# Optimization experiments

Hardware: AMD Instinct MI355X
Metric: run time of the kernel (lower is better)

The kernel has to match this reference:

```python
import jax, jax.numpy as jnp
import numpy as np

N_NODES = 100000
N_EDGES = 600000
DIMS = [128, 64, 32, 16, 9]  # in_channels -> conv1 -> conv2 -> conv3 -> n_classes


def _sage_layer(x, src, dst, w_l, w_r, b, n_nodes):
    # PyG SAGEConv (mean aggr): out = lin_l(mean_{j in N(i)} x_j) + lin_r(x_i)
    msgs = x[src]                                               # [E, F] gather
    agg = jax.ops.segment_sum(msgs, dst, num_segments=n_nodes)  # [N, F]
    deg = jax.ops.segment_sum(jnp.ones((src.shape[0], 1), x.dtype), dst,
                              num_segments=n_nodes)             # [N, 1]
    agg = agg / jnp.maximum(deg, 1.0)                           # mean over neighbors
    return agg @ w_l + x @ w_r + b                              # lin_l has bias, lin_r does not


def setup_inputs() -> dict:
    key = jax.random.key(0)
    ks = jax.random.split(key, 16)
    inp = {
        'embedding': jax.random.normal(ks[0], (N_NODES, DIMS[0]), dtype=jnp.float32),
        'edge_index': jax.random.randint(ks[1], (2, N_EDGES), 0, N_NODES, dtype=jnp.int32),
        'edge_attr': jax.random.uniform(ks[2], (N_EDGES,), dtype=jnp.float32),
    }
    for i in range(4):
        fin, fout = DIMS[i], DIMS[i + 1]
        s = 1.0 / np.sqrt(fin)
        inp[f'w_l{i}'] = jax.random.uniform(ks[3 + 3 * i], (fin, fout), minval=-s, maxval=s, dtype=jnp.float32)
        inp[f'w_r{i}'] = jax.random.uniform(ks[4 + 3 * i], (fin, fout), minval=-s, maxval=s, dtype=jnp.float32)
        inp[f'b{i}'] = jax.random.uniform(ks[5 + 3 * i], (fout,), minval=-s, maxval=s, dtype=jnp.float32)
    return inp


def reference(embedding, edge_index, edge_attr,
              w_l0, w_r0, b0, w_l1, w_r1, b1,
              w_l2, w_r2, b2, w_l3, w_r3, b3):
    # edge_attr is accepted but unused: PyG SAGEConv does not consume edge weights.
    # Dropout evaluated in inference mode (identity) for a deterministic reference.
    src, dst = edge_index[0], edge_index[1]
    n = embedding.shape[0]
    x = jax.nn.relu(_sage_layer(embedding, src, dst, w_l0, w_r0, b0, n))
    x = jax.nn.relu(_sage_layer(x, src, dst, w_l1, w_r1, b1, n))
    x = jax.nn.relu(_sage_layer(x, src, dst, w_l2, w_r2, b2, n))
    x = _sage_layer(x, src, dst, w_l3, w_r3, b3, n)
    return x
```

## Files before the change

kernel.cpp:

```cpp
#include <hip/hip_runtime.h>
#include <hip/hip_bf16.h>


#define BLK 256


__global__ void hist_kernel(const int* __restrict__ dst, int* __restrict__ deg, int e) {
    int t = blockIdx.x * blockDim.x + threadIdx.x;
    if (t < e) atomicAdd(&deg[dst[t]], 1);
}

__global__ void scan1_kernel(const int* __restrict__ deg, int* __restrict__ excl,
                             int* __restrict__ bsums, int n) {
    __shared__ int sm[256];
    int base = blockIdx.x * 1024;
    int t = threadIdx.x;
    int v[4];
    int s = 0;
    #pragma unroll
    for (int j = 0; j < 4; j++) {
        int i = base + t * 4 + j;
        v[j] = (i < n) ? deg[i] : 0;
        s += v[j];
    }
    sm[t] = s;
    __syncthreads();
    for (int off = 1; off < 256; off <<= 1) {
        int x = (t >= off) ? sm[t - off] : 0;
        __syncthreads();
        sm[t] += x;
        __syncthreads();
    }
    int excl_t = sm[t] - s;
    if (t == 255) bsums[blockIdx.x] = sm[255];
    int run = excl_t;
    #pragma unroll
    for (int j = 0; j < 4; j++) {
        int i = base + t * 4 + j;
        if (i < n) excl[i] = run;
        run += v[j];
    }
}

__global__ void scan2_kernel(int* __restrict__ bsums, int nb) {
    __shared__ int sm[256];
    int t = threadIdx.x;
    int v = (t < nb) ? bsums[t] : 0;
    sm[t] = v;
    __syncthreads();
    for (int off = 1; off < 256; off <<= 1) {
        int x = (t >= off) ? sm[t - off] : 0;
        __syncthreads();
        sm[t] += x;
        __syncthreads();
    }
    if (t < nb) bsums[t] = sm[t] - v;
}

__global__ void scan3_kernel(const int* __restrict__ deg, int* __restrict__ row_start,
                             const int* __restrict__ bsums, int* __restrict__ cursor,
                             float* __restrict__ inv_deg, int n, int e) {
    int t = blockIdx.x * blockDim.x + threadIdx.x;
    if (t < n) {
        int rs = row_start[t] + bsums[t >> 10];
        row_start[t] = rs;
        cursor[t] = rs;
        int d = deg[t];
        inv_deg[t] = 1.0f / (float)(d > 1 ? d : 1);
    }
    if (t == 0) row_start[n] = e;
}

__global__ void scatter_kernel(const int* __restrict__ src, const int* __restrict__ dst,
                               int* __restrict__ cursor, int* __restrict__ ssrc, int e) {
    int t = blockIdx.x * blockDim.x + threadIdx.x;
    if (t < e) {
        int p = atomicAdd(&cursor[dst[t]], 1);
        ssrc[p] = src[t];
    }
}


template <int FIN, int FOUT, int BM, int KC, int TM, int TN, int THREADS>
__global__ void lin_tiled3(const float* __restrict__ x, const float* __restrict__ wl,
                           const float* __restrict__ wr, const float* __restrict__ b,
                           float* __restrict__ y, float* __restrict__ z, int n) {
    constexpr int PAD = 4;
    constexpr int CPR = FOUT / TN;
    constexpr int XLOADS = (BM * KC) / (THREADS * 4);
    static_assert(THREADS == (BM / TM) * CPR, "thread shape mismatch");
    __shared__ float xT[KC][BM + PAD];

    const int tid = threadIdx.x;
    const int r = tid / CPR;
    const int c = tid % CPR;
    const int m0 = r * TM;
    const int f0 = c * TN;
    const int nodeBase = blockIdx.x * BM;

    int nodeIdx[XLOADS], kkIdx[XLOADS];
    bool inb[XLOADS];
    #pragma unroll
    for (int l = 0; l < XLOADS; l++) {
        int idx = (l * THREADS + tid) * 4;
        nodeIdx[l] = idx / KC;
        kkIdx[l] = idx % KC;
        inb[l] = (nodeBase + nodeIdx[l]) < n;
    }

    float4 xreg[XLOADS];
    #pragma unroll
    for (int l = 0; l < XLOADS; l++) {
        float4 v = {0.f, 0.f, 0.f, 0.f};
        if (inb[l]) v = *(const float4*)(x + (size_t)(nodeBase + nodeIdx[l]) * FIN + kkIdx[l]);
        xreg[l] = v;
    }

    float accy[TM][TN] = {};
    float accz[TM][TN] = {};

    constexpr int NCHUNK = FIN / KC;
    for (int ch = 0; ch < NCHUNK; ch++) {
        #pragma unroll
        for (int l = 0; l < XLOADS; l++) {
            xT[kkIdx[l] + 0][nodeIdx[l]] = xreg[l].x;
            xT[kkIdx[l] + 1][nodeIdx[l]] = xreg[l].y;
            xT[kkIdx[l] + 2][nodeIdx[l]] = xreg[l].z;
            xT[kkIdx[l] + 3][nodeIdx[l]] = xreg[l].w;
        }
        __syncthreads();
        if (ch + 1 < NCHUNK) {
            int k0n = (ch + 1) * KC;
            #pragma unroll
            for (int l = 0; l < XLOADS; l++) {
                float4 v = {0.f, 0.f, 0.f, 0.f};
                if (inb[l]) v = *(const float4*)(x + (size_t)(nodeBase + nodeIdx[l]) * FIN + k0n + kkIdx[l]);
                xreg[l] = v;
            }
        }
        const int k0 = ch * KC;
        #pragma unroll 8
        for (int k = 0; k < KC; k++) {
            float a[TM];
            #pragma unroll
            for (int i = 0; i < TM; i += 4) *(float4*)&a[i] = *(const float4*)&xT[k][m0 + i];
            float4 blv = *(const float4*)(wl + (size_t)(k0 + k) * FOUT + f0);
            float4 brv = *(const float4*)(wr + (size_t)(k0 + k) * FOUT + f0);
            float bl[4] = {blv.x, blv.y, blv.z, blv.w};
            float br[4] = {brv.x, brv.y, brv.z, brv.w};
            #pragma unroll
            for (int i = 0; i < TM; i++)
                #pragma unroll
                for (int j = 0; j < TN; j++) {
                    accy[i][j] = fmaf(a[i], bl[j], accy[i][j]);
                    accz[i][j] = fmaf(a[i], br[j], accz[i][j]);
                }
        }
        __syncthreads();
    }

    float4 bv = *(const float4*)(b + f0);
    float bias[4] = {bv.x, bv.y, bv.z, bv.w};
    #pragma unroll
    for (int i = 0; i < TM; i++) {
        int gn = nodeBase + m0 + i;
        if (gn < n) {
            #pragma unroll
            for (int j = 0; j < TN; j += 4) {
                float4 vy = {accy[i][j], accy[i][j+1], accy[i][j+2], accy[i][j+3]};
                float4 vz = {accz[i][j] + bias[j], accz[i][j+1] + bias[j+1],
                             accz[i][j+2] + bias[j+2], accz[i][j+3] + bias[j+3]};
                *(float4*)(y + (size_t)gn * FOUT + f0 + j) = vy;
                *(float4*)(z + (size_t)gn * FOUT + f0 + j) = vz;
            }
        }
    }
}

template <int FIN, int FOUT>
__global__ void lin_naive(const float* __restrict__ x, const float* __restrict__ wl,
                          const float* __restrict__ wr, const float* __restrict__ b,
                          float* __restrict__ y, float* __restrict__ z, int n) {
    int t = blockIdx.x * blockDim.x + threadIdx.x;
    int node = t / FOUT;
    int f = t % FOUT;
    if (node >= n) return;
    const float* xr = x + (size_t)node * FIN;
    float accy = 0.f, accz = 0.f;
    #pragma unroll
    for (int k = 0; k < FIN; k++) {
        float xv = xr[k];
        accy = fmaf(xv, wl[k * FOUT + f], accy);
        accz = fmaf(xv, wr[k * FOUT + f], accz);
    }
    y[(size_t)node * FOUT + f] = accy;
    z[(size_t)node * FOUT + f] = accz + b[f];
}


template <int FOUT, bool RELU>
__global__ void agg4_kernel(const float4* __restrict__ y4, const int* __restrict__ row_start,
                            const int* __restrict__ ssrc, const float* __restrict__ inv_deg,
                            float4* __restrict__ out4, int n) {
    constexpr int Q = FOUT / 4;
    int t = blockIdx.x * blockDim.x + threadIdx.x;
    int node = t / Q;
    int q = t % Q;
    if (node >= n) return;
    int e0 = row_start[node];
    int e1 = row_start[node + 1];
    float4 s = {0.f, 0.f, 0.f, 0.f};
    int e = e0;
    for (; e + 3 < e1; e += 4) {
        int sn0 = ssrc[e];
        int sn1 = ssrc[e + 1];
        int sn2 = ssrc[e + 2];
        int sn3 = ssrc[e + 3];
        float4 v0 = y4[(size_t)sn0 * Q + q];
        float4 v1 = y4[(size_t)sn1 * Q + q];
        float4 v2 = y4[(size_t)sn2 * Q + q];
        float4 v3 = y4[(size_t)sn3 * Q + q];
        s.x += v0.x + v1.x + v2.x + v3.x;
        s.y += v0.y + v1.y + v2.y + v3.y;
        s.z += v0.z + v1.z + v2.z + v3.z;
        s.w += v0.w + v1.w + v2.w + v3.w;
    }
    if (e + 1 < e1) {
        int sn0 = ssrc[e];
        int sn1 = ssrc[e + 1];
        float4 v0 = y4[(size_t)sn0 * Q + q];
        float4 v1 = y4[(size_t)sn1 * Q + q];
        s.x += v0.x + v1.x; s.y += v0.y + v1.y;
        s.z += v0.z + v1.z; s.w += v0.w + v1.w;
        e += 2;
    }
    if (e < e1) {
        int sn = ssrc[e];
        float4 v = y4[(size_t)sn * Q + q];
        s.x += v.x; s.y += v.y; s.z += v.z; s.w += v.w;
    }
    float id = inv_deg[node];
    float4 o = out4[(size_t)node * Q + q];
    o.x += s.x * id; o.y += s.y * id; o.z += s.z * id; o.w += s.w * id;
    if (RELU) {
        o.x = fmaxf(o.x, 0.f); o.y = fmaxf(o.y, 0.f);
        o.z = fmaxf(o.z, 0.f); o.w = fmaxf(o.w, 0.f);
    }
    out4[(size_t)node * Q + q] = o;
}

template <int FOUT, bool RELU>
__global__ void agg_kernel(const float* __restrict__ y, const int* __restrict__ row_start,
                           const int* __restrict__ ssrc, const float* __restrict__ inv_deg,
                           float* __restrict__ out, int n) {
    int t = blockIdx.x * blockDim.x + threadIdx.x;
    int node = t / FOUT;
    int f = t % FOUT;
    if (node >= n) return;
    int e0 = row_start[node];
    int e1 = row_start[node + 1];
    float s = 0.f;
    int e = e0;
    for (; e + 3 < e1; e += 4) {
        int sn0 = ssrc[e];
        int sn1 = ssrc[e + 1];
        int sn2 = ssrc[e + 2];
        int sn3 = ssrc[e + 3];
        float v0 = y[(size_t)sn0 * FOUT + f];
        float v1 = y[(size_t)sn1 * FOUT + f];
        float v2 = y[(size_t)sn2 * FOUT + f];
        float v3 = y[(size_t)sn3 * FOUT + f];
        s += (v0 + v1) + (v2 + v3);
    }
    for (; e < e1; e++) s += y[(size_t)ssrc[e] * FOUT + f];
    float v = out[(size_t)node * FOUT + f] + s * inv_deg[node];
    if (RELU) v = fmaxf(v, 0.f);
    out[(size_t)node * FOUT + f] = v;
}


static inline int cdiv(int a, int b) { return (a + b - 1) / b; }

extern "C" void kernel_launch(void* const* d_in, const int* in_sizes, int n_in,
                              void* d_out, int out_size, void* d_ws, size_t ws_size,
                              hipStream_t stream) {
    const float* emb  = (const float*)d_in[0];
    const int*   eidx = (const int*)d_in[1];
    const float* wl0 = (const float*)d_in[3];
    const float* wr0 = (const float*)d_in[4];
    const float* b0  = (const float*)d_in[5];
    const float* wl1 = (const float*)d_in[6];
    const float* wr1 = (const float*)d_in[7];
    const float* b1  = (const float*)d_in[8];
    const float* wl2 = (const float*)d_in[9];
    const float* wr2 = (const float*)d_in[10];
    const float* b2  = (const float*)d_in[11];
    const float* wl3 = (const float*)d_in[12];
    const float* wr3 = (const float*)d_in[13];
    const float* b3  = (const float*)d_in[14];

    const int n = in_sizes[0] / 128;
    const int e = in_sizes[1] / 2;
    const int* src = eidx;
    const int* dst = eidx + e;

    char* ws = (char*)d_ws;
    size_t off = 0;
    auto alloc = [&](size_t bytes) -> void* {
        void* p = ws + off;
        off = (off + bytes + 255) & ~(size_t)255;
        return p;
    };
    int*   deg       = (int*)alloc((size_t)n * 4);
    float* inv_deg   = (float*)alloc((size_t)n * 4);
    int*   row_start = (int*)alloc(((size_t)n + 1) * 4);
    int*   cursor    = (int*)alloc((size_t)n * 4);
    int*   bsums     = (int*)alloc(1024 * 4);
    int*   ssrc      = (int*)alloc((size_t)e * 4);
    float* Y         = (float*)alloc((size_t)n * 64 * 4);
    float* xA        = (float*)alloc((size_t)n * 64 * 4);
    float* xB        = (float*)alloc((size_t)n * 32 * 4);
    (void)ws_size;

    hipMemsetAsync(deg, 0, (size_t)n * 4, stream);
    hist_kernel<<<cdiv(e, BLK), BLK, 0, stream>>>(dst, deg, e);
    int nchunks = cdiv(n, 1024);
    scan1_kernel<<<nchunks, 256, 0, stream>>>(deg, row_start, bsums, n);
    scan2_kernel<<<1, 256, 0, stream>>>(bsums, nchunks);
    scan3_kernel<<<cdiv(n, BLK), BLK, 0, stream>>>(deg, row_start, bsums, cursor, inv_deg, n, e);
    scatter_kernel<<<cdiv(e, BLK), BLK, 0, stream>>>(src, dst, cursor, ssrc, e);

    float* out = (float*)d_out;

    lin_tiled3<128, 64, 128, 32, 8, 4, 256><<<cdiv(n, 128), 256, 0, stream>>>(emb, wl0, wr0, b0, Y, xA, n);
    agg4_kernel<64, true><<<cdiv(n * 16, BLK), BLK, 0, stream>>>((const float4*)Y, row_start, ssrc, inv_deg, (float4*)xA, n);

    lin_tiled3<64, 32, 64, 32, 4, 4, 128><<<cdiv(n, 64), 128, 0, stream>>>(xA, wl1, wr1, b1, Y, xB, n);
    agg4_kernel<32, true><<<cdiv(n * 8, BLK), BLK, 0, stream>>>((const float4*)Y, row_start, ssrc, inv_deg, (float4*)xB, n);

    lin_naive<32, 16><<<cdiv(n * 16, BLK), BLK, 0, stream>>>(xB, wl2, wr2, b2, Y, xA, n);
    agg4_kernel<16, true><<<cdiv(n * 4, BLK), BLK, 0, stream>>>((const float4*)Y, row_start, ssrc, inv_deg, (float4*)xA, n);

    lin_naive<16, 9><<<cdiv(n * 9, BLK), BLK, 0, stream>>>(xA, wl3, wr3, b3, Y, out, n);
    agg_kernel<9, false><<<cdiv(n * 9, BLK), BLK, 0, stream>>>(Y, row_start, ssrc, inv_deg, out, n);
}
```

Baseline: 408.3 us.

## Use direct global-to-LDS async loads with double buffering in dense layer kernels

Replaces the register-staged transposed shared-memory tile in the two large linear kernels with __builtin_amdgcn_global_load_lds copies into a double-buffered row-major LDS tile, prefetching the next K chunk while computing the current one. Reads of x from LDS become per-row float4 loads instead of transposed column reads. The second layer now uses 128-node blocks with 256 threads, and launch bounds are fixed to one block per CU hint. The change is meant to cut VGPR staging and the transpose stores, but it risks LDS bank conflicts on row-major reads and relies on implicit ordering of the async LDS loads. Out-of-range rows are simply skipped rather than zero-filled, which leaves stale LDS data that only feeds accumulators for rows that are never stored.

Measured after the change: 417.9 us. 2.4% more time.

```diff
diff --git a/kernel.cpp b/kernel.cpp
--- a/kernel.cpp
+++ b/kernel.cpp
@@ -3,6 +3,11 @@
 
 
 #define BLK 256
+
+#define GLOAD_LDS16(gptr, lptr)                                              \
+    __builtin_amdgcn_global_load_lds(                                        \
+        (const __attribute__((address_space(1))) void*)(gptr),               \
+        (__attribute__((address_space(3))) void*)(lptr), 16, 0, 0)
 
 
 __global__ void hist_kernel(const int* __restrict__ dst, int* __restrict__ deg, int e) {
@@ -81,98 +86,88 @@
 }
 
 
-template <int FIN, int FOUT, int BM, int KC, int TM, int TN, int THREADS>
-__global__ void lin_tiled3(const float* __restrict__ x, const float* __restrict__ wl,
-                           const float* __restrict__ wr, const float* __restrict__ b,
-                           float* __restrict__ y, float* __restrict__ z, int n) {
-    constexpr int PAD = 4;
+template <int FIN, int FOUT, int BM, int KC, int TM, int THREADS>
+__global__ __launch_bounds__(THREADS, 1)
+void lin_glds(const float* __restrict__ x, const float* __restrict__ wl,
+              const float* __restrict__ wr, const float* __restrict__ b,
+              float* __restrict__ y, float* __restrict__ z, int n) {
+    constexpr int TN = 4;
     constexpr int CPR = FOUT / TN;
-    constexpr int XLOADS = (BM * KC) / (THREADS * 4);
     static_assert(THREADS == (BM / TM) * CPR, "thread shape mismatch");
-    __shared__ float xT[KC][BM + PAD];
+    constexpr int SLOTS = BM * KC / 4;
+    constexpr int LPT = SLOTS / THREADS;
+    constexpr int SPR = KC / 4;
+    constexpr int NCH = FIN / KC;
+    __shared__ float xs[2][BM * KC];
 
     const int tid = threadIdx.x;
+    const int wave = tid >> 6;
     const int r = tid / CPR;
     const int c = tid % CPR;
     const int m0 = r * TM;
-    const int f0 = c * TN;
     const int nodeBase = blockIdx.x * BM;
-
-    int nodeIdx[XLOADS], kkIdx[XLOADS];
-    bool inb[XLOADS];
-    #pragma unroll
-    for (int l = 0; l < XLOADS; l++) {
-        int idx = (l * THREADS + tid) * 4;
-        nodeIdx[l] = idx / KC;
-        kkIdx[l] = idx % KC;
-        inb[l] = (nodeBase + nodeIdx[l]) < n;
-    }
-
-    float4 xreg[XLOADS];
-    #pragma unroll
-    for (int l = 0; l < XLOADS; l++) {
-        float4 v = {0.f, 0.f, 0.f, 0.f};
-        if (inb[l]) v = *(const float4*)(x + (size_t)(nodeBase + nodeIdx[l]) * FIN + kkIdx[l]);
-        xreg[l] = v;
-    }
+    const float4* wl4 = (const float4*)wl;
+    const float4* wr4 = (const float4*)wr;
+
+    auto stage = [&](int buf, int ch) {
+        #pragma unroll
+        for (int l = 0; l < LPT; l++) {
+            int s = l * THREADS + tid;
+            int node = s / SPR;
+            int kq = s % SPR;
+            const float* g = x + (size_t)(nodeBase + node) * FIN + ch * KC + kq * 4;
+            float* lbase = &xs[buf][(size_t)(l * THREADS + wave * 64) * 4];
+            if (nodeBase + node < n) GLOAD_LDS16(g, lbase);
+        }
+    };
+
+    stage(0, 0);
 
     float accy[TM][TN] = {};
     float accz[TM][TN] = {};
 
-    constexpr int NCHUNK = FIN / KC;
-    for (int ch = 0; ch < NCHUNK; ch++) {
+    __syncthreads();
+    for (int ch = 0; ch < NCH; ch++) {
+        const int cur = ch & 1;
+        if (ch + 1 < NCH) stage(cur ^ 1, ch + 1);
         #pragma unroll
-        for (int l = 0; l < XLOADS; l++) {
-            xT[kkIdx[l] + 0][nodeIdx[l]] = xreg[l].x;
-            xT[kkIdx[l] + 1][nodeIdx[l]] = xreg[l].y;
-            xT[kkIdx[l] + 2][nodeIdx[l]] = xreg[l].z;
-            xT[kkIdx[l] + 3][nodeIdx[l]] = xreg[l].w;
-        }
-        __syncthreads();
-        if (ch + 1 < NCHUNK) {
-            int k0n = (ch + 1) * KC;
+        for (int k4 = 0; k4 < KC / 4; k4++) {
+            float4 a4[TM];
             #pragma unroll
-            for (int l = 0; l < XLOADS; l++) {
-                float4 v = {0.f, 0.f, 0.f, 0.f};
-                if (inb[l]) v = *(const float4*)(x + (size_t)(nodeBase + nodeIdx[l]) * FIN + k0n + kkIdx[l]);
-                xreg[l] = v;
+            for (int i = 0; i < TM; i++)
+                a4[i] = *(const float4*)&xs[cur][(m0 + i) * KC + k4 * 4];
+            #pragma unroll
+            for (int kk = 0; kk < 4; kk++) {
+                int k = ch * KC + k4 * 4 + kk;
+                float4 blv = wl4[(size_t)k * CPR + c];
+                float4 brv = wr4[(size_t)k * CPR + c];
+                #pragma unroll
+                for (int i = 0; i < TM; i++) {
+                    float av = ((const float*)&a4[i])[kk];
+                    accy[i][0] = fmaf(av, blv.x, accy[i][0]);
+                    accy[i][1] = fmaf(av, blv.y, accy[i][1]);
+                    accy[i][2] = fmaf(av, blv.z, accy[i][2]);
+                    accy[i][3] = fmaf(av, blv.w, accy[i][3]);
+                    accz[i][0] = fmaf(av, brv.x, accz[i][0]);
+                    accz[i][1] = fmaf(av, brv.y, accz[i][1]);
+                    accz[i][2] = fmaf(av, brv.z, accz[i][2]);
+                    accz[i][3] = fmaf(av, brv.w, accz[i][3]);
+                }
             }
         }
-        const int k0 = ch * KC;
-        #pragma unroll 8
-        for (int k = 0; k < KC; k++) {
-            float a[TM];
-            #pragma unroll
-            for (int i = 0; i < TM; i += 4) *(float4*)&a[i] = *(const float4*)&xT[k][m0 + i];
-            float4 blv = *(const float4*)(wl + (size_t)(k0 + k) * FOUT + f0);
-            float4 brv = *(const float4*)(wr + (size_t)(k0 + k) * FOUT + f0);
-            float bl[4] = {blv.x, blv.y, blv.z, blv.w};
-            float br[4] = {brv.x, brv.y, brv.z, brv.w};
-            #pragma unroll
-            for (int i = 0; i < TM; i++)
-                #pragma unroll
-                for (int j = 0; j < TN; j++) {
-                    accy[i][j] = fmaf(a[i], bl[j], accy[i][j]);
-                    accz[i][j] = fmaf(a[i], br[j], accz[i][j]);
-                }
-        }
-        __syncthreads();
-    }
-
-    float4 bv = *(const float4*)(b + f0);
-    float bias[4] = {bv.x, bv.y, bv.z, bv.w};
+        __syncthreads();
+    }
+
+    float4 bv = *(const float4*)(b + c * 4);
     #pragma unroll
     for (int i = 0; i < TM; i++) {
         int gn = nodeBase + m0 + i;
         if (gn < n) {
-            #pragma unroll
-            for (int j = 0; j < TN; j += 4) {
-                float4 vy = {accy[i][j], accy[i][j+1], accy[i][j+2], accy[i][j+3]};
-                float4 vz = {accz[i][j] + bias[j], accz[i][j+1] + bias[j+1],
-                             accz[i][j+2] + bias[j+2], accz[i][j+3] + bias[j+3]};
-                *(float4*)(y + (size_t)gn * FOUT + f0 + j) = vy;
-                *(float4*)(z + (size_t)gn * FOUT + f0 + j) = vz;
-            }
+            float4 vy = {accy[i][0], accy[i][1], accy[i][2], accy[i][3]};
+            float4 vz = {accz[i][0] + bv.x, accz[i][1] + bv.y,
+                         accz[i][2] + bv.z, accz[i][3] + bv.w};
+            *(float4*)(y + (size_t)gn * FOUT + c * 4) = vy;
+            *(float4*)(z + (size_t)gn * FOUT + c * 4) = vz;
         }
     }
 }
@@ -332,10 +327,10 @@
 
     float* out = (float*)d_out;
 
-    lin_tiled3<128, 64, 128, 32, 8, 4, 256><<<cdiv(n, 128), 256, 0, stream>>>(emb, wl0, wr0, b0, Y, xA, n);
+    lin_glds<128, 64, 128, 32, 8, 256><<<cdiv(n, 128), 256, 0, stream>>>(emb, wl0, wr0, b0, Y, xA, n);
     agg4_kernel<64, true><<<cdiv(n * 16, BLK), BLK, 0, stream>>>((const float4*)Y, row_start, ssrc, inv_deg, (float4*)xA, n);
 
-    lin_tiled3<64, 32, 64, 32, 4, 4, 128><<<cdiv(n, 64), 128, 0, stream>>>(xA, wl1, wr1, b1, Y, xB, n);
+    lin_glds<64, 32, 128, 32, 4, 256><<<cdiv(n, 128), 256, 0, stream>>>(xA, wl1, wr1, b1, Y, xB, n);
     agg4_kernel<32, true><<<cdiv(n * 8, BLK), BLK, 0, stream>>>((const float4*)Y, row_start, ssrc, inv_deg, (float4*)xB, n);
 
     lin_naive<32, 16><<<cdiv(n * 16, BLK), BLK, 0, stream>>>(xB, wl2, wr2, b2, Y, xA, n);
```
